# Performance work log

Hardware: AMD Instinct MI355X
Metric: run time of the kernel (lower is better)

Reference implementation:

```python
import jax, jax.numpy as jnp
import numpy as np


def setup_inputs() -> dict:
    key = jax.random.key(0)
    ks = jax.random.split(key, 4)
    B, T, D, H, E = 4, 2048, 1024, 4096, 8
    s = 0.02
    x = jax.random.normal(ks[0], (B, T, D), dtype=jnp.float32)
    Wr = jax.random.normal(ks[1], (D, E), dtype=jnp.float32) * s
    br = jnp.zeros((E,), dtype=jnp.float32)
    W1 = jax.random.normal(ks[2], (E, D, H), dtype=jnp.float32) * s
    b1 = jnp.zeros((E, H), dtype=jnp.float32)
    W2 = jax.random.normal(ks[3], (E, H, D), dtype=jnp.float32) * s
    b2 = jnp.zeros((E, D), dtype=jnp.float32)
    return {"x": x, "Wr": Wr, "br": br, "W1": W1, "b1": b1, "W2": W2, "b2": b2}


def reference(x, Wr, br, W1, b1, W2, b2):
    # Router: top-1 selection
    logits = jnp.einsum('btd,de->bte', x, Wr) + br            # [B,T,E]
    probs = jax.nn.softmax(logits, axis=-1)                   # [B,T,E]
    expert_idx = jnp.argmax(probs, axis=-1)                   # [B,T] int
    E = W1.shape[0]
    onehot = jax.nn.one_hot(expert_idx, E, dtype=x.dtype)     # [B,T,E]
    # Dense grouped-MLP over all experts, then combine with one-hot routing.
    # h: [B,E,T,H]
    h = jax.nn.relu(jnp.einsum('btd,edh->beth', x, W1) + b1[None, :, None, :])
    y = jnp.einsum('beth,ehd->betd', h, W2) + b2[None, :, None, :]  # [B,E,T,D]
    out = jnp.einsum('bte,betd->btd', onehot, y)              # [B,T,D]
    return out, probs, expert_idx
```

## Files before the change

kernel.cpp:

```cpp
#include <hip/hip_runtime.h>

#define NTOK 8192
#define DD 1024
#define HH 4096
#define EE 8
#define MAXBLK 72

typedef __attribute__((ext_vector_type(8))) short bf16x8;
typedef __attribute__((ext_vector_type(4))) float f32x4;

__device__ __forceinline__ unsigned short f2bf(float f) {
  unsigned u = __builtin_bit_cast(unsigned, f);
  u += 0x7fffu + ((u >> 16) & 1u);
  return (unsigned short)(u >> 16);
}

union Pack8 {
  unsigned short u[8];
  uint4 v;
};

__device__ __forceinline__ void gload_lds16(const void* g, void* l) {
  __builtin_amdgcn_global_load_lds(
      (const __attribute__((address_space(1))) unsigned int*)g,
      (__attribute__((address_space(3))) unsigned int*)l, 16, 0, 0);
}

__device__ __forceinline__ void trcvt_body(const float* __restrict__ src0,
                                           unsigned short* __restrict__ dst0,
                                           int R, int C, int r0, int c0,
                                           unsigned short* t) {
  const int tid = threadIdx.x;
  const float* src = src0 + (size_t)r0 * C + c0;
  unsigned short* dst = dst0 + (size_t)c0 * R + r0;
#pragma unroll
  for (int it = 0; it < 4; ++it) {
    const int r = it * 16 + (tid >> 4), c4 = (tid & 15) * 4;
    const float4 v = *reinterpret_cast<const float4*>(src + (size_t)r * C + c4);
    t[r * 66 + c4 + 0] = f2bf(v.x);
    t[r * 66 + c4 + 1] = f2bf(v.y);
    t[r * 66 + c4 + 2] = f2bf(v.z);
    t[r * 66 + c4 + 3] = f2bf(v.w);
  }
  __syncthreads();
#pragma unroll
  for (int it = 0; it < 2; ++it) {
    const int cc = it * 32 + (tid >> 3), r8 = (tid & 7) * 8;
    Pack8 p;
#pragma unroll
    for (int j = 0; j < 8; ++j) p.u[j] = t[(r8 + j) * 66 + cc];
    *reinterpret_cast<uint4*>(dst + (size_t)cc * R + r8) = p.v;
  }
}

__global__ __launch_bounds__(256) void k_rtr1(
    const float* __restrict__ x, const float* __restrict__ Wr,
    const float* __restrict__ br, float* __restrict__ probs,
    float* __restrict__ idxf, int* __restrict__ idxi,
    unsigned short* __restrict__ xb,
    const float* __restrict__ W1, unsigned short* __restrict__ W1t) {
  __shared__ __align__(16) unsigned short SH[64 * 66];
  const int bid = blockIdx.x;
  if (bid < NTOK / 4) {
    const int lane = threadIdx.x & 63;
    const int token = bid * 4 + (threadIdx.x >> 6);
    const float* xr = x + (size_t)token * DD;

    float acc[EE];
#pragma unroll
    for (int e = 0; e < EE; ++e) acc[e] = 0.f;

#pragma unroll
    for (int i = 0; i < 4; ++i) {
      const int d0 = i * 256 + lane * 4;
      const float4 xv = *reinterpret_cast<const float4*>(xr + d0);
      union { unsigned short u[4]; uint2 v; } pk;
      pk.u[0] = f2bf(xv.x); pk.u[1] = f2bf(xv.y);
      pk.u[2] = f2bf(xv.z); pk.u[3] = f2bf(xv.w);
      *reinterpret_cast<uint2*>(xb + (size_t)token * DD + d0) = pk.v;
      const float xs[4] = {xv.x, xv.y, xv.z, xv.w};
#pragma unroll
      for (int j = 0; j < 4; ++j) {
        const float xd = xs[j];
        const float4 w0 = *reinterpret_cast<const float4*>(Wr + (size_t)(d0 + j) * EE);
        const float4 w1 = *reinterpret_cast<const float4*>(Wr + (size_t)(d0 + j) * EE + 4);
        acc[0] += xd * w0.x; acc[1] += xd * w0.y; acc[2] += xd * w0.z; acc[3] += xd * w0.w;
        acc[4] += xd * w1.x; acc[5] += xd * w1.y; acc[6] += xd * w1.z; acc[7] += xd * w1.w;
      }
    }
#pragma unroll
    for (int s = 32; s > 0; s >>= 1) {
#pragma unroll
      for (int e = 0; e < EE; ++e) acc[e] += __shfl_xor(acc[e], s, 64);
    }

    float lg[EE];
#pragma unroll
    for (int e = 0; e < EE; ++e) lg[e] = acc[e] + br[e];

    int best = 0;
    float bv = lg[0];
#pragma unroll
    for (int e = 1; e < EE; ++e) {
      if (lg[e] > bv) { bv = lg[e]; best = e; }
    }
    float p[EE], s = 0.f;
#pragma unroll
    for (int e = 0; e < EE; ++e) { p[e] = expf(lg[e] - bv); s += p[e]; }
    const float inv = 1.f / s;

    if (lane == 0) {
#pragma unroll
      for (int e = 0; e < EE; ++e) probs[(size_t)token * EE + e] = p[e] * inv;
      idxf[token] = (float)best;
      idxi[token] = best;
    }
  } else {
    const int t = bid - NTOK / 4;
    const int e = t >> 10;
    const int rem = t & 1023;
    const int c0 = (rem & 63) * 64;
    const int r0 = (rem >> 6) * 64;
    trcvt_body(W1 + (size_t)e * DD * HH, W1t + (size_t)e * DD * HH, DD, HH, r0, c0, SH);
  }
}

__global__ __launch_bounds__(512) void k_compact(const int* __restrict__ idxi,
                                                 int* __restrict__ cnt,
                                                 int* __restrict__ off,
                                                 int* __restrict__ sorted,
                                                 int* __restrict__ meta) {
  __shared__ int sidx[NTOK];
  __shared__ int scnt[EE], soff[EE];
  const int tid = threadIdx.x;
  for (int i = tid; i < NTOK; i += 512) sidx[i] = idxi[i];
  __syncthreads();
  const int w = tid >> 6, lane = tid & 63;
  if (w < EE) {
    int c = 0;
    for (int i = 0; i < NTOK / 64; ++i) {
      unsigned long long m = __ballot(sidx[i * 64 + lane] == w);
      c += __popcll(m);
    }
    if (lane == 0) scnt[w] = c;
  }
  __syncthreads();
  if (tid == 0) {
    int s = 0;
    for (int e = 0; e < EE; ++e) { soff[e] = s; s += scnt[e]; }
    int nb = 0;
    for (int e = 0; e < EE; ++e) {
      const int nmb = (scnt[e] + 127) >> 7;
      for (int m = 0; m < nmb; ++m) {
        meta[16 + nb] = e;
        meta[96 + nb] = m << 7;
        ++nb;
      }
    }
    meta[0] = nb;
  }
  __syncthreads();
  if (w < EE) {
    int base = soff[w];
    const unsigned long long ltmask = (1ull << lane) - 1ull;
    for (int i = 0; i < NTOK / 64; ++i) {
      const int tok = i * 64 + lane;
      const bool f = (sidx[tok] == w);
      unsigned long long m = __ballot(f);
      if (f) {
        int r = __popcll(m & ltmask);
        sorted[base + r] = tok;
      }
      base += __popcll(m);
    }
    if (lane == 0) { cnt[w] = scnt[w]; off[w] = soff[w]; }
  }
}

__global__ __launch_bounds__(256) void k_trcvt64(const float* __restrict__ in,
                                                 unsigned short* __restrict__ outp,
                                                 int R, int C) {
  __shared__ unsigned short t[64 * 66];
  const int e = blockIdx.z;
  trcvt_body(in + (size_t)e * R * C, outp + (size_t)e * R * C, R, C,
             blockIdx.y * 64, blockIdx.x * 64, t);
}

__global__ __launch_bounds__(256) void k_g1tr2(
    const unsigned short* __restrict__ xb, const unsigned short* __restrict__ W1t,
    const float* __restrict__ b1, const int* __restrict__ meta,
    const int* __restrict__ cnt, const int* __restrict__ off,
    const int* __restrict__ sorted, unsigned short* __restrict__ h,
    const float* __restrict__ W2, unsigned short* __restrict__ W2t) {
  __shared__ __align__(16) unsigned short SH[2 * 128 * 64];
  if (blockIdx.y >= MAXBLK) {
    const int t = (blockIdx.y - MAXBLK) * 32 + blockIdx.x;
    const int e = t >> 10;
    const int rem = t & 1023;
    const int c0 = (rem & 15) * 64;
    const int r0 = (rem >> 4) * 64;
    trcvt_body(W2 + (size_t)e * HH * DD, W2t + (size_t)e * HH * DD, HH, DD, r0, c0, SH);
    return;
  }
  const int bid = blockIdx.y;
  if (bid >= meta[0]) return;
  const int e = meta[16 + bid];
  const int m0 = meta[96 + bid];
  const int c = cnt[e], base = off[e];
  const int n0 = blockIdx.x * 128;

  unsigned short* Al = SH;
  unsigned short* Bl = SH + 128 * 64;

  const int tid = threadIdx.x, l = tid & 63, w = tid >> 6;

  const unsigned short* aptr[4];
  const unsigned short* bptr[4];
  int soff4[4];
#pragma unroll
  for (int i = 0; i < 4; ++i) {
    const int r = i * 32 + w * 8 + (l >> 3);
    const int swz = ((l & 7) ^ (r & 7)) * 8;
    int ar = m0 + r; if (ar >= c) ar = c - 1;
    const int tok = sorted[base + ar];
    aptr[i] = xb + (size_t)tok * DD + swz;
    bptr[i] = W1t + ((size_t)e * HH + n0 + r) * DD + swz;
    soff4[i] = r * 64 + (l & 7) * 8;
  }

  const int lr = l & 15, lg = l >> 4;
  const int wr = w >> 1, wc = w & 1;
  int aoff[4], boff[4], asw[4], bsw[4];
#pragma unroll
  for (int m = 0; m < 4; ++m) {
    int row = wr * 64 + m * 16 + lr;
    aoff[m] = row * 64; asw[m] = row & 7;
    row = wc * 64 + m * 16 + lr;
    boff[m] = row * 64; bsw[m] = row & 7;
  }

  f32x4 acc[4][4];
#pragma unroll
  for (int m = 0; m < 4; ++m)
#pragma unroll
    for (int n = 0; n < 4; ++n) acc[m][n] = {0.f, 0.f, 0.f, 0.f};

  for (int k0 = 0; k0 < DD; k0 += 64) {
    __syncthreads();
#pragma unroll
    for (int i = 0; i < 4; ++i) gload_lds16(aptr[i] + k0, &Al[soff4[i]]);
#pragma unroll
    for (int i = 0; i < 4; ++i) gload_lds16(bptr[i] + k0, &Bl[soff4[i]]);
    __syncthreads();
#pragma unroll
    for (int ks = 0; ks < 2; ++ks) {
      bf16x8 af[4], bv[4];
#pragma unroll
      for (int m = 0; m < 4; ++m)
        af[m] = *reinterpret_cast<const bf16x8*>(&Al[aoff[m] + (((ks * 4 + lg) ^ asw[m]) * 8)]);
#pragma unroll
      for (int n = 0; n < 4; ++n)
        bv[n] = *reinterpret_cast<const bf16x8*>(&Bl[boff[n] + (((ks * 4 + lg) ^ bsw[n]) * 8)]);
#pragma unroll
      for (int m = 0; m < 4; ++m)
#pragma unroll
        for (int n = 0; n < 4; ++n)
          acc[m][n] = __builtin_amdgcn_mfma_f32_16x16x32_bf16(af[m], bv[n], acc[m][n], 0, 0, 0);
    }
  }

  const int valid = c - m0;
#pragma unroll
  for (int m = 0; m < 4; ++m) {
#pragma unroll
    for (int rr = 0; rr < 4; ++rr) {
      const int tr = wr * 64 + m * 16 + lg * 4 + rr;
      if (tr < valid) {
        const size_t row = (size_t)(base + m0 + tr);
#pragma unroll
        for (int n = 0; n < 4; ++n) {
          const int col = n0 + wc * 64 + n * 16 + lr;
          const float v = acc[m][n][rr] + b1[e * HH + col];
          h[row * HH + col] = f2bf(fmaxf(v, 0.f));
        }
      }
    }
  }
}

template <int KH>
__global__ __launch_bounds__(256) void k_gemm2s(
    const unsigned short* __restrict__ h, const unsigned short* __restrict__ W2t,
    const float* __restrict__ b2, const int* __restrict__ meta,
    const int* __restrict__ cnt, const int* __restrict__ off,
    const int* __restrict__ sorted, float* __restrict__ out,
    float* __restrict__ scr) {
  const int bid = blockIdx.y;
  if (bid >= meta[0]) return;
  const int e = meta[16 + bid];
  const int m0 = meta[96 + bid];
  const int c = cnt[e], base = off[e];
  const int n0 = blockIdx.x * 64;
  const int kh = (KH == 2) ? blockIdx.z : 0;
  const int kbase = kh * (HH / KH);

  __shared__ __align__(16) unsigned short Al0[128 * 64];
  __shared__ __align__(16) unsigned short Al1[128 * 64];
  __shared__ __align__(16) unsigned short Bl0[64 * 64];
  __shared__ __align__(16) unsigned short Bl1[64 * 64];

  const int tid = threadIdx.x, l = tid & 63, w = tid >> 6;

  const unsigned short* aptr[4];
  const unsigned short* bptr[2];
  int asoff[4], bsoff[2];
#pragma unroll
  for (int i = 0; i < 4; ++i) {
    const int r = i * 32 + w * 8 + (l >> 3);
    const int swz = ((l & 7) ^ (r & 7)) * 8;
    int ar = m0 + r; if (ar >= c) ar = c - 1;
    aptr[i] = h + (size_t)(base + ar) * HH + kbase + swz;
    asoff[i] = r * 64 + (l & 7) * 8;
  }
#pragma unroll
  for (int i = 0; i < 2; ++i) {
    const int r = i * 32 + w * 8 + (l >> 3);
    const int swz = ((l & 7) ^ (r & 7)) * 8;
    bptr[i] = W2t + ((size_t)e * DD + n0 + r) * HH + kbase + swz;
    bsoff[i] = r * 64 + (l & 7) * 8;
  }

  const int lr = l & 15, lg = l >> 4;
  const int wr = w >> 1, wc = w & 1;
  int aoff[4], boff[2], asw[4], bsw[2];
#pragma unroll
  for (int m = 0; m < 4; ++m) {
    const int row = wr * 64 + m * 16 + lr;
    aoff[m] = row * 64; asw[m] = row & 7;
  }
#pragma unroll
  for (int n = 0; n < 2; ++n) {
    const int row = wc * 32 + n * 16 + lr;
    boff[n] = row * 64; bsw[n] = row & 7;
  }

  f32x4 acc[4][2];
#pragma unroll
  for (int m = 0; m < 4; ++m)
#pragma unroll
    for (int n = 0; n < 2; ++n) acc[m][n] = {0.f, 0.f, 0.f, 0.f};

  for (int k0 = 0; k0 < HH / KH; k0 += 128) {
    __syncthreads();
#pragma unroll
    for (int i = 0; i < 4; ++i) gload_lds16(aptr[i] + k0, &Al0[asoff[i]]);
#pragma unroll
    for (int i = 0; i < 4; ++i) gload_lds16(aptr[i] + k0 + 64, &Al1[asoff[i]]);
#pragma unroll
    for (int i = 0; i < 2; ++i) gload_lds16(bptr[i] + k0, &Bl0[bsoff[i]]);
#pragma unroll
    for (int i = 0; i < 2; ++i) gload_lds16(bptr[i] + k0 + 64, &Bl1[bsoff[i]]);
    __syncthreads();
#pragma unroll
    for (int ks = 0; ks < 2; ++ks) {
      bf16x8 af[4], bv[2];
#pragma unroll
      for (int m = 0; m < 4; ++m)
        af[m] = *reinterpret_cast<const bf16x8*>(&Al0[aoff[m] + (((ks * 4 + lg) ^ asw[m]) * 8)]);
#pragma unroll
      for (int n = 0; n < 2; ++n)
        bv[n] = *reinterpret_cast<const bf16x8*>(&Bl0[boff[n] + (((ks * 4 + lg) ^ bsw[n]) * 8)]);
#pragma unroll
      for (int m = 0; m < 4; ++m)
#pragma unroll
        for (int n = 0; n < 2; ++n)
          acc[m][n] = __builtin_amdgcn_mfma_f32_16x16x32_bf16(af[m], bv[n], acc[m][n], 0, 0, 0);
    }
#pragma unroll
    for (int ks = 0; ks < 2; ++ks) {
      bf16x8 af[4], bv[2];
#pragma unroll
      for (int m = 0; m < 4; ++m)
        af[m] = *reinterpret_cast<const bf16x8*>(&Al1[aoff[m] + (((ks * 4 + lg) ^ asw[m]) * 8)]);
#pragma unroll
      for (int n = 0; n < 2; ++n)
        bv[n] = *reinterpret_cast<const bf16x8*>(&Bl1[boff[n] + (((ks * 4 + lg) ^ bsw[n]) * 8)]);
#pragma unroll
      for (int m = 0; m < 4; ++m)
#pragma unroll
        for (int n = 0; n < 2; ++n)
          acc[m][n] = __builtin_amdgcn_mfma_f32_16x16x32_bf16(af[m], bv[n], acc[m][n], 0, 0, 0);
    }
  }

  float* dst = (KH == 2 && blockIdx.z == 1) ? scr : out;
  const int valid = c - m0;
#pragma unroll
  for (int m = 0; m < 4; ++m) {
#pragma unroll
    for (int rr = 0; rr < 4; ++rr) {
      const int tr = wr * 64 + m * 16 + lg * 4 + rr;
      if (tr < valid) {
        const int token = sorted[base + m0 + tr];
#pragma unroll
        for (int n = 0; n < 2; ++n) {
          const int col = n0 + wc * 32 + n * 16 + lr;
          float v = acc[m][n][rr];
          if (KH == 1) v += b2[e * DD + col];
          dst[(size_t)token * DD + col] = v;
        }
      }
    }
  }
}

__global__ __launch_bounds__(256) void k_reduce2(float* __restrict__ out,
                                                 const float* __restrict__ scr,
                                                 const float* __restrict__ b2,
                                                 const int* __restrict__ idxi) {
  const size_t f = (size_t)blockIdx.x * 256 + threadIdx.x;
  const int token = (int)(f >> 8);
  const int d4 = ((int)f & 255) * 4;
  const int e = idxi[token];
  const float4 a = *reinterpret_cast<const float4*>(out + f * 4);
  const float4 b = *reinterpret_cast<const float4*>(scr + f * 4);
  const float4 bb = *reinterpret_cast<const float4*>(b2 + (size_t)e * DD + d4);
  float4 r;
  r.x = a.x + b.x + bb.x;
  r.y = a.y + b.y + bb.y;
  r.z = a.z + b.z + bb.z;
  r.w = a.w + b.w + bb.w;
  *reinterpret_cast<float4*>(out + f * 4) = r;
}

extern "C" void kernel_launch(void* const* d_in, const int* in_sizes, int n_in,
                              void* d_out, int out_size, void* d_ws, size_t ws_size,
                              hipStream_t stream) {
  const float* x  = (const float*)d_in[0];
  const float* Wr = (const float*)d_in[1];
  const float* br = (const float*)d_in[2];
  const float* W1 = (const float*)d_in[3];
  const float* b1 = (const float*)d_in[4];
  const float* W2 = (const float*)d_in[5];
  const float* b2 = (const float*)d_in[6];

  float* out   = (float*)d_out;
  float* probs = out + (size_t)NTOK * DD;
  float* idxf  = probs + (size_t)NTOK * EE;

  char* ws = (char*)d_ws;
  int* cnt    = (int*)(ws + 0);
  int* off    = (int*)(ws + 64);
  int* meta   = (int*)(ws + 128);
  int* idxi   = (int*)(ws + 1024);
  int* sorted = (int*)(ws + 33792);

  const size_t OFF_XB   = 66560;
  const size_t OFF_W1T  = OFF_XB + (size_t)NTOK * DD * 2;
  const size_t OFF_H    = OFF_W1T + (size_t)EE * DD * HH * 2;
  const size_t OFF_SCR  = OFF_H + (size_t)NTOK * HH * 2;
  const size_t OFF_W2TB = OFF_SCR + (size_t)NTOK * DD * 4;
  const size_t NEED_SPLIT = OFF_W2TB;
  const size_t NEED_BIG   = OFF_W2TB + (size_t)EE * DD * HH * 2;

  unsigned short* xb  = (unsigned short*)(ws + OFF_XB);
  unsigned short* W1t = (unsigned short*)(ws + OFF_W1T);
  unsigned short* h   = (unsigned short*)(ws + OFF_H);
  float*          scr = (float*)(ws + OFF_SCR);

  k_rtr1<<<NTOK / 4 + 8192, 256, 0, stream>>>(x, Wr, br, probs, idxf, idxi, xb, W1, W1t);
  k_compact<<<1, 512, 0, stream>>>(idxi, cnt, off, sorted, meta);

  if (ws_size >= NEED_BIG) {
    unsigned short* W2t = (unsigned short*)(ws + OFF_W2TB);
    k_g1tr2<<<dim3(HH / 128, MAXBLK + 256), 256, 0, stream>>>(
        xb, W1t, b1, meta, cnt, off, sorted, h, W2, W2t);
    k_gemm2s<2><<<dim3(DD / 64, MAXBLK, 2), 256, 0, stream>>>(
        h, W2t, b2, meta, cnt, off, sorted, out, scr);
    k_reduce2<<<(NTOK * DD) / (256 * 4), 256, 0, stream>>>(out, scr, b2, idxi);
  } else if (ws_size >= NEED_SPLIT) {
    unsigned short* W2t = (unsigned short*)(ws + OFF_XB);
    k_g1tr2<<<dim3(HH / 128, MAXBLK), 256, 0, stream>>>(
        xb, W1t, b1, meta, cnt, off, sorted, h, W2, W2t);
    k_trcvt64<<<dim3(DD / 64, HH / 64, EE), 256, 0, stream>>>(W2, W2t, HH, DD);
    k_gemm2s<2><<<dim3(DD / 64, MAXBLK, 2), 256, 0, stream>>>(
        h, W2t, b2, meta, cnt, off, sorted, out, scr);
    k_reduce2<<<(NTOK * DD) / (256 * 4), 256, 0, stream>>>(out, scr, b2, idxi);
  } else {
    unsigned short* W2t = (unsigned short*)(ws + OFF_XB);
    k_g1tr2<<<dim3(HH / 128, MAXBLK), 256, 0, stream>>>(
        xb, W1t, b1, meta, cnt, off, sorted, h, W2, W2t);
    k_trcvt64<<<dim3(DD / 64, HH / 64, EE), 256, 0, stream>>>(W2, W2t, HH, DD);
    k_gemm2s<1><<<dim3(DD / 64, MAXBLK, 1), 256, 0, stream>>>(
        h, W2t, b2, meta, cnt, off, sorted, out, scr);
  }
}
```

Baseline: 373.8 us.

## Replace split-K second GEMM with single-wave 64x64-tile full-K kernel

The compaction step now also builds a 64-row block schedule. The second expert GEMM in the large-workspace path switches from a 2-way split-K kernel plus a reduction kernel to one-wavefront blocks on 64x64 output tiles. Each block covers the full H dimension with double-buffered direct-to-LDS loads and writes scattered outputs with bias directly. This removes the scratch write, the reduce kernel launch and its memory traffic. In exchange each block is small (64 threads) with a long serial K loop, and staging reuse per block is lower.

```diff
diff --git a/kernel.cpp b/kernel.cpp
--- a/kernel.cpp
+++ b/kernel.cpp
@@ -5,6 +5,7 @@
 #define HH 4096
 #define EE 8
 #define MAXBLK 72
+#define MAXBLK64 136
 
 typedef __attribute__((ext_vector_type(8))) short bf16x8;
 typedef __attribute__((ext_vector_type(4))) float f32x4;
@@ -158,6 +159,16 @@
       }
     }
     meta[0] = nb;
+    int nb64 = 0;
+    for (int e = 0; e < EE; ++e) {
+      const int nmb = (scnt[e] + 63) >> 6;
+      for (int m = 0; m < nmb; ++m) {
+        meta[176 + nb64] = e;
+        meta[320 + nb64] = m << 6;
+        ++nb64;
+      }
+    }
+    meta[1] = nb64;
   }
   __syncthreads();
   if (w < EE) {
@@ -282,6 +293,117 @@
           const int col = n0 + wc * 64 + n * 16 + lr;
           const float v = acc[m][n][rr] + b1[e * HH + col];
           h[row * HH + col] = f2bf(fmaxf(v, 0.f));
+        }
+      }
+    }
+  }
+}
+
+__global__ __launch_bounds__(64) void k_gemm2w(
+    const unsigned short* __restrict__ h, const unsigned short* __restrict__ W2t,
+    const float* __restrict__ b2, const int* __restrict__ meta,
+    const int* __restrict__ cnt, const int* __restrict__ off,
+    const int* __restrict__ sorted, float* __restrict__ out) {
+  const int bid = blockIdx.y;
+  if (bid >= meta[1]) return;
+  const int e = meta[176 + bid];
+  const int m0 = meta[320 + bid];
+  const int c = cnt[e], base = off[e];
+  const int n0 = blockIdx.x * 64;
+
+  __shared__ __align__(16) unsigned short A0[64 * 64];
+  __shared__ __align__(16) unsigned short A1[64 * 64];
+  __shared__ __align__(16) unsigned short B0[64 * 64];
+  __shared__ __align__(16) unsigned short B1[64 * 64];
+
+  const int l = threadIdx.x;
+
+  const unsigned short* aptr[8];
+  const unsigned short* bptr[8];
+  int soff[8];
+#pragma unroll
+  for (int i = 0; i < 8; ++i) {
+    const int r = i * 8 + (l >> 3);
+    const int swz = ((l & 7) ^ (r & 7)) * 8;
+    int ar = m0 + r; if (ar >= c) ar = c - 1;
+    aptr[i] = h + (size_t)(base + ar) * HH + swz;
+    bptr[i] = W2t + ((size_t)e * DD + n0 + r) * HH + swz;
+    soff[i] = r * 64 + (l & 7) * 8;
+  }
+
+  const int lr = l & 15, lg = l >> 4;
+  int foff[4], fsw[4];
+#pragma unroll
+  for (int m = 0; m < 4; ++m) {
+    const int row = m * 16 + lr;
+    foff[m] = row * 64; fsw[m] = row & 7;
+  }
+
+  f32x4 acc[4][4];
+#pragma unroll
+  for (int m = 0; m < 4; ++m)
+#pragma unroll
+    for (int n = 0; n < 4; ++n) acc[m][n] = {0.f, 0.f, 0.f, 0.f};
+
+#define STGW(Ab, Bb, kk)                                                    \
+  {                                                                         \
+    _Pragma("unroll") for (int i = 0; i < 8; ++i)                           \
+        gload_lds16(aptr[i] + (kk), &Ab[soff[i]]);                          \
+    _Pragma("unroll") for (int i = 0; i < 8; ++i)                           \
+        gload_lds16(bptr[i] + (kk), &Bb[soff[i]]);                          \
+  }
+
+#define CMPW(Ab, Bb)                                                        \
+  {                                                                         \
+    _Pragma("unroll") for (int ks = 0; ks < 2; ++ks) {                      \
+      bf16x8 af[4], bv[4];                                                  \
+      _Pragma("unroll") for (int m = 0; m < 4; ++m)                         \
+          af[m] = *reinterpret_cast<const bf16x8*>(                         \
+              &Ab[foff[m] + (((ks * 4 + lg) ^ fsw[m]) * 8)]);               \
+      _Pragma("unroll") for (int n = 0; n < 4; ++n)                         \
+          bv[n] = *reinterpret_cast<const bf16x8*>(                         \
+              &Bb[foff[n] + (((ks * 4 + lg) ^ fsw[n]) * 8)]);               \
+      _Pragma("unroll") for (int m = 0; m < 4; ++m)                         \
+          _Pragma("unroll") for (int n = 0; n < 4; ++n)                     \
+              acc[m][n] = __builtin_amdgcn_mfma_f32_16x16x32_bf16(          \
+                  af[m], bv[n], acc[m][n], 0, 0, 0);                        \
+    }                                                                       \
+  }
+
+  STGW(A0, B0, 0);
+  STGW(A1, B1, 64);
+
+#pragma unroll 1
+  for (int t = 0; t < 62; t += 2) {
+    asm volatile("s_waitcnt vmcnt(16)" ::: "memory");
+    CMPW(A0, B0);
+    __builtin_amdgcn_sched_barrier(0);
+    STGW(A0, B0, (t + 2) * 64);
+    asm volatile("s_waitcnt vmcnt(16)" ::: "memory");
+    CMPW(A1, B1);
+    __builtin_amdgcn_sched_barrier(0);
+    STGW(A1, B1, (t + 3) * 64);
+  }
+  asm volatile("s_waitcnt vmcnt(16)" ::: "memory");
+  CMPW(A0, B0);
+  asm volatile("s_waitcnt vmcnt(0)" ::: "memory");
+  CMPW(A1, B1);
+
+#undef STGW
+#undef CMPW
+
+  const int valid = c - m0;
+#pragma unroll
+  for (int m = 0; m < 4; ++m) {
+#pragma unroll
+    for (int rr = 0; rr < 4; ++rr) {
+      const int tr = m * 16 + lg * 4 + rr;
+      if (tr < valid) {
+        const int token = sorted[base + m0 + tr];
+#pragma unroll
+        for (int n = 0; n < 4; ++n) {
+          const int col = n0 + n * 16 + lr;
+          out[(size_t)token * DD + col] = acc[m][n][rr] + b2[e * DD + col];
         }
       }
     }
@@ -452,10 +574,10 @@
   int* cnt    = (int*)(ws + 0);
   int* off    = (int*)(ws + 64);
   int* meta   = (int*)(ws + 128);
-  int* idxi   = (int*)(ws + 1024);
-  int* sorted = (int*)(ws + 33792);
-
-  const size_t OFF_XB   = 66560;
+  int* idxi   = (int*)(ws + 2176);
+  int* sorted = (int*)(ws + 34944);
+
+  const size_t OFF_XB   = 67712;
   const size_t OFF_W1T  = OFF_XB + (size_t)NTOK * DD * 2;
   const size_t OFF_H    = OFF_W1T + (size_t)EE * DD * HH * 2;
   const size_t OFF_SCR  = OFF_H + (size_t)NTOK * HH * 2;
@@ -475,9 +597,8 @@
     unsigned short* W2t = (unsigned short*)(ws + OFF_W2TB);
     k_g1tr2<<<dim3(HH / 128, MAXBLK + 256), 256, 0, stream>>>(
         xb, W1t, b1, meta, cnt, off, sorted, h, W2, W2t);
-    k_gemm2s<2><<<dim3(DD / 64, MAXBLK, 2), 256, 0, stream>>>(
-        h, W2t, b2, meta, cnt, off, sorted, out, scr);
-    k_reduce2<<<(NTOK * DD) / (256 * 4), 256, 0, stream>>>(out, scr, b2, idxi);
+    k_gemm2w<<<dim3(DD / 64, MAXBLK64), 64, 0, stream>>>(
+        h, W2t, b2, meta, cnt, off, sorted, out);
   } else if (ws_size >= NEED_SPLIT) {
     unsigned short* W2t = (unsigned short*)(ws + OFF_XB);
     k_g1tr2<<<dim3(HH / 128, MAXBLK), 256, 0, stream>>>(
```

Result: slower. 405.4 us (+8.5%).

## Double-buffer LDS tiles in second expert GEMM to overlap loads with MFMA

Applied to the files above, without the earlier changes.

Restructures the second grouped GEMM's K loop from a load-all-then-compute scheme into a ping-pong double buffer over 64-wide K tiles. The next tile's global-to-LDS loads are issued before computing on the current buffer, with explicit vmcnt waits and raw barriers in place of __syncthreads. The goal is to hide global load latency behind MFMA work. The trade-off is more fragile synchronisation that depends on the exact count of outstanding loads.

```diff
diff --git a/kernel.cpp b/kernel.cpp
--- a/kernel.cpp
+++ b/kernel.cpp
@@ -289,7 +289,7 @@
 }
 
 template <int KH>
-__global__ __launch_bounds__(256) void k_gemm2s(
+__global__ __launch_bounds__(256) void k_gemm2d(
     const unsigned short* __restrict__ h, const unsigned short* __restrict__ W2t,
     const float* __restrict__ b2, const int* __restrict__ meta,
     const int* __restrict__ cnt, const int* __restrict__ off,
@@ -304,10 +304,10 @@
   const int kh = (KH == 2) ? blockIdx.z : 0;
   const int kbase = kh * (HH / KH);
 
-  __shared__ __align__(16) unsigned short Al0[128 * 64];
-  __shared__ __align__(16) unsigned short Al1[128 * 64];
-  __shared__ __align__(16) unsigned short Bl0[64 * 64];
-  __shared__ __align__(16) unsigned short Bl1[64 * 64];
+  __shared__ __align__(16) unsigned short A0[128 * 64];
+  __shared__ __align__(16) unsigned short A1[128 * 64];
+  __shared__ __align__(16) unsigned short B0[64 * 64];
+  __shared__ __align__(16) unsigned short B1[64 * 64];
 
   const int tid = threadIdx.x, l = tid & 63, w = tid >> 6;
 
@@ -350,48 +350,58 @@
 #pragma unroll
     for (int n = 0; n < 2; ++n) acc[m][n] = {0.f, 0.f, 0.f, 0.f};
 
-  for (int k0 = 0; k0 < HH / KH; k0 += 128) {
-    __syncthreads();
-#pragma unroll
-    for (int i = 0; i < 4; ++i) gload_lds16(aptr[i] + k0, &Al0[asoff[i]]);
-#pragma unroll
-    for (int i = 0; i < 4; ++i) gload_lds16(aptr[i] + k0 + 64, &Al1[asoff[i]]);
-#pragma unroll
-    for (int i = 0; i < 2; ++i) gload_lds16(bptr[i] + k0, &Bl0[bsoff[i]]);
-#pragma unroll
-    for (int i = 0; i < 2; ++i) gload_lds16(bptr[i] + k0 + 64, &Bl1[bsoff[i]]);
-    __syncthreads();
-#pragma unroll
-    for (int ks = 0; ks < 2; ++ks) {
-      bf16x8 af[4], bv[2];
-#pragma unroll
-      for (int m = 0; m < 4; ++m)
-        af[m] = *reinterpret_cast<const bf16x8*>(&Al0[aoff[m] + (((ks * 4 + lg) ^ asw[m]) * 8)]);
-#pragma unroll
-      for (int n = 0; n < 2; ++n)
-        bv[n] = *reinterpret_cast<const bf16x8*>(&Bl0[boff[n] + (((ks * 4 + lg) ^ bsw[n]) * 8)]);
-#pragma unroll
-      for (int m = 0; m < 4; ++m)
-#pragma unroll
-        for (int n = 0; n < 2; ++n)
-          acc[m][n] = __builtin_amdgcn_mfma_f32_16x16x32_bf16(af[m], bv[n], acc[m][n], 0, 0, 0);
-    }
-#pragma unroll
-    for (int ks = 0; ks < 2; ++ks) {
-      bf16x8 af[4], bv[2];
-#pragma unroll
-      for (int m = 0; m < 4; ++m)
-        af[m] = *reinterpret_cast<const bf16x8*>(&Al1[aoff[m] + (((ks * 4 + lg) ^ asw[m]) * 8)]);
-#pragma unroll
-      for (int n = 0; n < 2; ++n)
-        bv[n] = *reinterpret_cast<const bf16x8*>(&Bl1[boff[n] + (((ks * 4 + lg) ^ bsw[n]) * 8)]);
-#pragma unroll
-      for (int m = 0; m < 4; ++m)
-#pragma unroll
-        for (int n = 0; n < 2; ++n)
-          acc[m][n] = __builtin_amdgcn_mfma_f32_16x16x32_bf16(af[m], bv[n], acc[m][n], 0, 0, 0);
-    }
-  }
+#define STG2(Ab, Bb, kk)                                                    \
+  {                                                                         \
+    _Pragma("unroll") for (int i = 0; i < 4; ++i)                           \
+        gload_lds16(aptr[i] + (kk), &Ab[asoff[i]]);                         \
+    _Pragma("unroll") for (int i = 0; i < 2; ++i)                           \
+        gload_lds16(bptr[i] + (kk), &Bb[bsoff[i]]);                         \
+  }
+
+#define CMP2(Ab, Bb)                                                        \
+  {                                                                         \
+    _Pragma("unroll") for (int ks = 0; ks < 2; ++ks) {                      \
+      bf16x8 af[4], bv[2];                                                  \
+      _Pragma("unroll") for (int m = 0; m < 4; ++m)                         \
+          af[m] = *reinterpret_cast<const bf16x8*>(                         \
+              &Ab[aoff[m] + (((ks * 4 + lg) ^ asw[m]) * 8)]);               \
+      _Pragma("unroll") for (int n = 0; n < 2; ++n)                         \
+          bv[n] = *reinterpret_cast<const bf16x8*>(                         \
+              &Bb[boff[n] + (((ks * 4 + lg) ^ bsw[n]) * 8)]);               \
+      _Pragma("unroll") for (int m = 0; m < 4; ++m)                         \
+          _Pragma("unroll") for (int n = 0; n < 2; ++n)                     \
+              acc[m][n] = __builtin_amdgcn_mfma_f32_16x16x32_bf16(          \
+                  af[m], bv[n], acc[m][n], 0, 0, 0);                        \
+    }                                                                       \
+  }
+
+  const int NT = (HH / KH) / 64;
+
+  STG2(A0, B0, 0);
+
+#pragma unroll 1
+  for (int t2 = 1; t2 + 1 < NT; t2 += 2) {
+    STG2(A1, B1, t2 * 64);
+    asm volatile("s_waitcnt vmcnt(6)" ::: "memory");
+    __builtin_amdgcn_s_barrier();
+    CMP2(A0, B0);
+    __builtin_amdgcn_s_barrier();
+    STG2(A0, B0, (t2 + 1) * 64);
+    asm volatile("s_waitcnt vmcnt(6)" ::: "memory");
+    __builtin_amdgcn_s_barrier();
+    CMP2(A1, B1);
+    __builtin_amdgcn_s_barrier();
+  }
+  STG2(A1, B1, (NT - 1) * 64);
+  asm volatile("s_waitcnt vmcnt(6)" ::: "memory");
+  __builtin_amdgcn_s_barrier();
+  CMP2(A0, B0);
+  asm volatile("s_waitcnt vmcnt(0)" ::: "memory");
+  __builtin_amdgcn_s_barrier();
+  CMP2(A1, B1);
+
+#undef STG2
+#undef CMP2
 
   float* dst = (KH == 2 && blockIdx.z == 1) ? scr : out;
   const int valid = c - m0;
@@ -475,7 +485,7 @@
     unsigned short* W2t = (unsigned short*)(ws + OFF_W2TB);
     k_g1tr2<<<dim3(HH / 128, MAXBLK + 256), 256, 0, stream>>>(
         xb, W1t, b1, meta, cnt, off, sorted, h, W2, W2t);
-    k_gemm2s<2><<<dim3(DD / 64, MAXBLK, 2), 256, 0, stream>>>(
+    k_gemm2d<2><<<dim3(DD / 64, MAXBLK, 2), 256, 0, stream>>>(
         h, W2t, b2, meta, cnt, off, sorted, out, scr);
     k_reduce2<<<(NTOK * DD) / (256 * 4), 256, 0, stream>>>(out, scr, b2, idxi);
   } else if (ws_size >= NEED_SPLIT) {
@@ -483,7 +493,7 @@
     k_g1tr2<<<dim3(HH / 128, MAXBLK), 256, 0, stream>>>(
         xb, W1t, b1, meta, cnt, off, sorted, h, W2, W2t);
     k_trcvt64<<<dim3(DD / 64, HH / 64, EE), 256, 0, stream>>>(W2, W2t, HH, DD);
-    k_gemm2s<2><<<dim3(DD / 64, MAXBLK, 2), 256, 0, stream>>>(
+    k_gemm2d<2><<<dim3(DD / 64, MAXBLK, 2), 256, 0, stream>>>(
         h, W2t, b2, meta, cnt, off, sorted, out, scr);
     k_reduce2<<<(NTOK * DD) / (256 * 4), 256, 0, stream>>>(out, scr, b2, idxi);
   } else {
@@ -491,7 +501,7 @@
     k_g1tr2<<<dim3(HH / 128, MAXBLK), 256, 0, stream>>>(
         xb, W1t, b1, meta, cnt, off, sorted, h, W2, W2t);
     k_trcvt64<<<dim3(DD / 64, HH / 64, EE), 256, 0, stream>>>(W2, W2t, HH, DD);
-    k_gemm2s<1><<<dim3(DD / 64, MAXBLK, 1), 256, 0, stream>>>(
+    k_gemm2d<1><<<dim3(DD / 64, MAXBLK, 1), 256, 0, stream>>>(
         h, W2t, b2, meta, cnt, off, sorted, out, scr);
   }
 }
```

Measured after the change: 372.4 us. Within noise of the previous version (-0.4%).
